# Performance work log

Hardware: AMD Instinct MI355X
Metric: run time of the kernel (lower is better)

Reference implementation:

```python
import jax, jax.numpy as jnp
import numpy as np

B, S, D = 4, 4096, 1024

def setup_inputs() -> dict:
    key = jax.random.key(0)
    kx, kq, kk, kv = jax.random.split(key, 4)
    x = jax.random.normal(kx, (B, S, D), dtype=jnp.float32)
    # nn.Linear weights, stored here as [d_in, d_out] so y = x @ W
    scale = 1.0 / np.sqrt(D)
    Wq = jax.random.normal(kq, (D, D), dtype=jnp.float32) * scale
    Wk = jax.random.normal(kk, (D, D), dtype=jnp.float32) * scale
    Wv = jax.random.normal(kv, (D, D), dtype=jnp.float32) * scale
    return {"x": x, "Wq": Wq, "Wk": Wk, "Wv": Wv}

def reference(x, Wq, Wk, Wv):
    b, n, d_in = x.shape
    d_out = Wk.shape[1]
    q = jnp.einsum('bnd,de->bne', x, Wq)
    k = jnp.einsum('bnd,de,->bne', x, Wk, 1.0)  # keys
    v = jnp.einsum('bnd,de->bne', x, Wv)
    # full causal attention: scores scaled by 1/sqrt(d_out) AFTER masking (matches source)
    scores = jnp.einsum('bqe,bke->bqk', q, k)
    causal = jnp.triu(jnp.ones((n, n), dtype=bool), k=1)  # True above diagonal -> masked
    scores = jnp.where(causal[None, :, :], -jnp.inf, scores)
    attn = jax.nn.softmax(scores / jnp.sqrt(jnp.asarray(d_out, scores.dtype)), axis=-1)
    # dropout p=0.0 (eval) -> identity
    return jnp.einsum('bqk,bke->bqe', attn, v)
```

## Files before the change

kernel.cpp:

```cpp
#include <hip/hip_runtime.h>
#include <hip/hip_bf16.h>

#define B_ 4
#define S_ 4096
#define D_ 1024
#define NT_ 32
#define PAIRS_ 528

typedef __attribute__((ext_vector_type(8))) short short8;
typedef __attribute__((ext_vector_type(4))) float f32x4;

__device__ __forceinline__ unsigned short f2bf(float f) {
    union { float f; unsigned u; } v; v.f = f;
    unsigned u = v.u;
    return (unsigned short)((u + 0x7fffu + ((u >> 16) & 1u)) >> 16);
}

__device__ __forceinline__ void gld_lds16(const unsigned short* g, unsigned short* l) {
    __builtin_amdgcn_global_load_lds((const __attribute__((address_space(1))) void*)g,
                                     (__attribute__((address_space(3))) void*)l, 16, 0, 0);
}

#define LGKM0 asm volatile("s_waitcnt lgkmcnt(0)" ::: "memory")
#define VM0   asm volatile("s_waitcnt vmcnt(0)" ::: "memory")
#define VM4   asm volatile("s_waitcnt vmcnt(4)" ::: "memory")
#define BAR   __builtin_amdgcn_s_barrier()
#define SB0   __builtin_amdgcn_sched_barrier(0)

__global__ __launch_bounds__(256) void prep_x(const float* __restrict__ x,
                                              unsigned short* __restrict__ xb) {
    size_t i = ((size_t)blockIdx.x * 256 + threadIdx.x) * 8;
    float4 a = *(const float4*)&x[i];
    float4 b = *(const float4*)&x[i + 4];
    unsigned u0 = (unsigned)f2bf(a.x) | ((unsigned)f2bf(a.y) << 16);
    unsigned u1 = (unsigned)f2bf(a.z) | ((unsigned)f2bf(a.w) << 16);
    unsigned u2 = (unsigned)f2bf(b.x) | ((unsigned)f2bf(b.y) << 16);
    unsigned u3 = (unsigned)f2bf(b.z) | ((unsigned)f2bf(b.w) << 16);
    uint4 val; val.x = u0; val.y = u1; val.z = u2; val.w = u3;
    *(uint4*)&xb[i] = val;
}

__global__ __launch_bounds__(256) void prep_w(const float* __restrict__ Wq,
                                              const float* __restrict__ Wk,
                                              const float* __restrict__ Wv,
                                              unsigned short* __restrict__ Wt) {
    __shared__ float ls[64 * 65];
    const int z = blockIdx.z;
    const float* __restrict__ W = (z == 0) ? Wq : (z == 1) ? Wk : Wv;
    unsigned short* __restrict__ Wtz = Wt + (size_t)z * D_ * D_;
    const int k0 = blockIdx.y * 64, n0 = blockIdx.x * 64;
    const int tid = threadIdx.x;
    #pragma unroll
    for (int i = 0; i < 16; ++i) {
        int lin = i * 256 + tid, r = lin >> 6, c = lin & 63;
        ls[r * 65 + c] = W[(size_t)(k0 + r) * D_ + n0 + c];
    }
    __syncthreads();
    #pragma unroll
    for (int i = 0; i < 16; ++i) {
        int lin = i * 256 + tid, r = lin >> 6, c = lin & 63;
        Wtz[(size_t)(n0 + r) * D_ + k0 + c] = f2bf(ls[c * 65 + r]);
    }
}

__global__ __launch_bounds__(512, 2) void qkv_gemm(
    const unsigned short* __restrict__ xb, const unsigned short* __restrict__ Wt,
    unsigned short* __restrict__ Q, unsigned short* __restrict__ K,
    unsigned short* __restrict__ Vt)
{
    __shared__ __align__(16) unsigned short ls[3 * 16384];

    const int z = blockIdx.z;
    const float scale = (z == 0) ? 0.03125f : 1.0f;

    const int lin = blockIdx.x;
    const int wg = (lin & 7) * 32 + (lin >> 3);
    const int m0 = (wg >> 2) * 256, n0 = (wg & 3) * 256;

    const int tid = threadIdx.x, lane = tid & 63, w = tid >> 6;
    const int wm = w >> 2, wn = w & 3;
    const int quad = lane >> 4, ln = lane & 15;

    const unsigned short* Ab = xb + (size_t)m0 * D_;
    const unsigned short* Bb = Wt + (size_t)z * D_ * D_ + (size_t)n0 * D_;

#define QKV_STAGE(kt, r)                                                          \
    {                                                                             \
        _Pragma("unroll")                                                         \
        for (int i_ = 0; i_ < 2; ++i_) {                                          \
            int g_ = tid + i_ * 512;                                              \
            int row_ = g_ >> 2;                                                   \
            int gs_ = (g_ & 3) ^ ((row_ >> 1) & 3);                               \
            gld_lds16(Ab + (size_t)row_ * D_ + (kt) * 32 + gs_ * 8,               \
                      ls + (r) * 16384 + g_ * 8);                                 \
            gld_lds16(Bb + (size_t)row_ * D_ + (kt) * 32 + gs_ * 8,               \
                      ls + (r) * 16384 + 8192 + g_ * 8);                          \
        }                                                                         \
    }

    f32x4 acc[8][4] = {};

#define QKV_BODY(r)                                                              \
    {                                                                            \
        const unsigned short* As_ = ls + (r) * 16384;                            \
        const unsigned short* Bs_ = As_ + 8192;                                  \
        short8 a_[8], b_[4];                                                     \
        _Pragma("unroll")                                                        \
        for (int mf_ = 0; mf_ < 8; ++mf_) {                                      \
            int row_ = wm * 128 + mf_ * 16 + ln;                                 \
            int g_ = quad ^ ((row_ >> 1) & 3);                                   \
            a_[mf_] = *(const short8*)&As_[row_ * 32 + g_ * 8];                  \
        }                                                                        \
        _Pragma("unroll")                                                        \
        for (int nf_ = 0; nf_ < 4; ++nf_) {                                      \
            int row_ = wn * 64 + nf_ * 16 + ln;                                  \
            int g_ = quad ^ ((row_ >> 1) & 3);                                   \
            b_[nf_] = *(const short8*)&Bs_[row_ * 32 + g_ * 8];                  \
        }                                                                        \
        __builtin_amdgcn_s_setprio(1);                                          \
        _Pragma("unroll")                                                        \
        for (int mf_ = 0; mf_ < 8; ++mf_)                                        \
            _Pragma("unroll")                                                    \
            for (int nf_ = 0; nf_ < 4; ++nf_)                                    \
                acc[mf_][nf_] = __builtin_amdgcn_mfma_f32_16x16x32_bf16(         \
                    a_[mf_], b_[nf_], acc[mf_][nf_], 0, 0, 0);                   \
        __builtin_amdgcn_s_setprio(0);                                          \
    }

#define QKV_STEP(t, r, rn, wcode)                                                \
    {                                                                            \
        if ((wcode) == 0) QKV_STAGE((t) + 2, rn)                                 \
        SB0;                                                                     \
        QKV_BODY(r)                                                              \
        LGKM0; SB0;                                                              \
        if ((wcode) == 0)      { VM4; SB0; BAR; SB0; }                           \
        else if ((wcode) == 1) { VM0; SB0; BAR; SB0; }                           \
    }

    QKV_STAGE(0, 0) QKV_STAGE(1, 1)
    VM4; SB0;
    BAR; SB0;

    #pragma unroll 1
    for (int tb = 0; tb < 30; tb += 3) {
        QKV_STEP(tb,     0, 2, 0)
        QKV_STEP(tb + 1, 1, 0, 0)
        QKV_STEP(tb + 2, 2, 1, 0)
    }
    QKV_STEP(30, 0, 0, 1)
    QKV_STEP(31, 1, 0, 2)

#undef QKV_STAGE
#undef QKV_BODY
#undef QKV_STEP

    if (z != 2) {
        unsigned short* __restrict__ Y = (z == 0) ? Q : K;
        #pragma unroll
        for (int mf = 0; mf < 8; ++mf)
            #pragma unroll
            for (int nf = 0; nf < 4; ++nf)
                #pragma unroll
                for (int rr = 0; rr < 4; ++rr) {
                    int row = m0 + wm * 128 + mf * 16 + quad * 4 + rr;
                    int col = n0 + wn * 64 + nf * 16 + ln;
                    Y[(size_t)row * D_ + col] = f2bf(acc[mf][nf][rr] * scale);
                }
    } else {
        BAR;
        unsigned int* U = (unsigned int*)ls + w * 2080;
        const int b_ = m0 >> 12;
        const int sbase = (m0 & 4095) + wm * 128;
        unsigned int* VtU = (unsigned int*)Vt;
        #pragma unroll
        for (int ch = 0; ch < 2; ++ch) {
            #pragma unroll
            for (int nfl = 0; nfl < 2; ++nfl) {
                int nf = ch * 2 + nfl;
                int el = nfl * 16 + ln;
                #pragma unroll
                for (int mf = 0; mf < 8; ++mf)
                    #pragma unroll
                    for (int pr = 0; pr < 2; ++pr) {
                        unsigned lo = f2bf(acc[mf][nf][2 * pr]);
                        unsigned hi = f2bf(acc[mf][nf][2 * pr + 1]);
                        U[el * 65 + mf * 8 + quad * 2 + pr] = lo | (hi << 16);
                    }
            }
            LGKM0; SB0;
            #pragma unroll 4
            for (int el = 0; el < 32; ++el) {
                unsigned v = U[el * 65 + lane];
                int eg = n0 + wn * 64 + ch * 32 + el;
                VtU[(((size_t)b_ * D_ + eg) * S_ + sbase) / 2 + lane] = v;
            }
            if (ch == 0) { LGKM0; SB0; }
        }
    }
}

__global__ __launch_bounds__(256, 3) void qk_pexp(
    const unsigned short* __restrict__ Q, const unsigned short* __restrict__ K,
    unsigned short* __restrict__ P, float* __restrict__ lpart)
{
    __shared__ __align__(16) unsigned short ls[3 * 8192];
    __shared__ float sml[2][128];

    const int l = blockIdx.x, b = blockIdx.y;
    const int r = l & 7;
    const int s = l >> 3;
    int qt, kt;
    if (s < r + 1)            { qt = r;      kt = s; }
    else if (s < 33)          { qt = 31 - r; kt = s - (r + 1); }
    else if (s < 42 + r)      { qt = 8 + r;  kt = s - 33; }
    else                      { qt = 23 - r; kt = s - (42 + r); }
    const int p = qt * (qt + 1) / 2 + kt;

    const int q0 = qt * 128, k0 = kt * 128;
    const int tid = threadIdx.x, lane = tid & 63, w = tid >> 6;
    const int wm = w >> 1, wn = w & 1, quad = lane >> 4, ln = lane & 15;
    const size_t base = (size_t)b * S_ * D_;

    const unsigned short* Qb = Q + base + (size_t)q0 * D_;
    const unsigned short* Kb = K + base + (size_t)k0 * D_;

#define QK_STAGE(kt_, r_)                                                         \
    {                                                                             \
        _Pragma("unroll")                                                         \
        for (int i_ = 0; i_ < 2; ++i_) {                                          \
            int g_ = tid + i_ * 256;                                              \
            int row_ = g_ >> 2;                                                   \
            int gs_ = (g_ & 3) ^ ((row_ >> 1) & 3);                               \
            gld_lds16(Qb + (size_t)row_ * D_ + (kt_) * 32 + gs_ * 8,              \
                      ls + (r_) * 8192 + g_ * 8);                                 \
            gld_lds16(Kb + (size_t)row_ * D_ + (kt_) * 32 + gs_ * 8,              \
                      ls + (r_) * 8192 + 4096 + g_ * 8);                          \
        }                                                                         \
    }

    f32x4 acc[4][4] = {};

#define QK_BODY(r_)                                                              \
    {                                                                            \
        const unsigned short* As_ = ls + (r_) * 8192;                            \
        const unsigned short* Bs_ = As_ + 4096;                                  \
        short8 a_[4], b_[4];                                                     \
        _Pragma("unroll")                                                        \
        for (int mf_ = 0; mf_ < 4; ++mf_) {                                      \
            int row_ = wm * 64 + mf_ * 16 + ln;                                  \
            int g_ = quad ^ ((row_ >> 1) & 3);                                   \
            a_[mf_] = *(const short8*)&As_[row_ * 32 + g_ * 8];                  \
        }                                                                        \
        _Pragma("unroll")                                                        \
        for (int nf_ = 0; nf_ < 4; ++nf_) {                                      \
            int row_ = wn * 64 + nf_ * 16 + ln;                                  \
            int g_ = quad ^ ((row_ >> 1) & 3);                                   \
            b_[nf_] = *(const short8*)&Bs_[row_ * 32 + g_ * 8];                  \
        }                                                                        \
        __builtin_amdgcn_s_setprio(1);                                          \
        _Pragma("unroll")                                                        \
        for (int mf_ = 0; mf_ < 4; ++mf_)                                        \
            _Pragma("unroll")                                                    \
            for (int nf_ = 0; nf_ < 4; ++nf_)                                    \
                acc[mf_][nf_] = __builtin_amdgcn_mfma_f32_16x16x32_bf16(         \
                    a_[mf_], b_[nf_], acc[mf_][nf_], 0, 0, 0);                   \
        __builtin_amdgcn_s_setprio(0);                                          \
    }

#define QK_STEP(t, r_, rn, wcode)                                                \
    {                                                                            \
        if ((wcode) == 0) QK_STAGE((t) + 2, rn)                                  \
        SB0;                                                                     \
        QK_BODY(r_)                                                              \
        LGKM0; SB0;                                                              \
        if ((wcode) == 0)      { VM4; SB0; BAR; SB0; }                           \
        else if ((wcode) == 1) { VM0; SB0; BAR; SB0; }                           \
    }

    QK_STAGE(0, 0) QK_STAGE(1, 1)
    VM4; SB0;
    BAR; SB0;

    #pragma unroll 1
    for (int tb = 0; tb < 30; tb += 3) {
        QK_STEP(tb,     0, 2, 0)
        QK_STEP(tb + 1, 1, 0, 0)
        QK_STEP(tb + 2, 2, 1, 0)
    }
    QK_STEP(30, 0, 0, 1)
    QK_STEP(31, 1, 0, 2)

#undef QK_STAGE
#undef QK_BODY
#undef QK_STEP

    const bool diag = (kt == qt);
    unsigned short* Pt = P + ((size_t)b * PAIRS_ + p) * (128 * 128);

    #pragma unroll
    for (int mf = 0; mf < 4; ++mf)
        #pragma unroll
        for (int rr = 0; rr < 4; ++rr) {
            int rowq = wm * 64 + mf * 16 + quad * 4 + rr;
            float lsum = 0.0f;
            #pragma unroll
            for (int nf = 0; nf < 4; ++nf) {
                int ckey = wn * 64 + nf * 16 + ln;
                float sc = acc[mf][nf][rr];
                float pe = (diag && ckey > rowq) ? 0.0f : __expf(fminf(sc, 60.0f));
                Pt[rowq * 128 + ckey] = f2bf(pe);
                lsum += pe;
            }
            #pragma unroll
            for (int off = 1; off < 16; off <<= 1)
                lsum += __shfl_xor(lsum, off);
            if (ln == 0) sml[wn][rowq] = lsum;
        }
    __syncthreads();

    if (tid < 128)
        lpart[((size_t)b * PAIRS_ + p) * 128 + tid] = sml[0][tid] + sml[1][tid];
}

__global__ __launch_bounds__(128) void merge_il(const float* __restrict__ lpart,
                                                float* __restrict__ il) {
    const int qt = blockIdx.x, b = blockIdx.y;
    const int row = threadIdx.x;
    const int pbase = qt * (qt + 1) / 2;
    float l = 0.0f;
    for (int kt = 0; kt <= qt; ++kt)
        l += lpart[((size_t)b * PAIRS_ + pbase + kt) * 128 + row];
    il[(size_t)b * S_ + qt * 128 + row] = 1.0f / l;
}

__global__ __launch_bounds__(256, 3) void pv_gemm(
    const unsigned short* __restrict__ P, const unsigned short* __restrict__ Vt,
    const float* __restrict__ il, float* __restrict__ O)
{
    __shared__ __align__(16) unsigned short ls[3 * 8192];

    const int bid = blockIdx.x;
    const int u  = (bid & 7) | ((bid >> 6) << 3);
    const int dt = (bid >> 3) & 7;
    const int pair = u & 15;
    const int b = u >> 4;
    const int d0 = dt * 128;
    const int tid = threadIdx.x, lane = tid & 63, w = tid >> 6;
    const int wm = w >> 1, wn = w & 1, quad = lane >> 4, ln = lane & 15;

    const unsigned short* Vtb = Vt + ((size_t)b * D_ + d0) * S_;

#define PV_STAGE(c_, r_)                                                          \
    {                                                                             \
        const unsigned short* Pt_ = Pbase + (size_t)((c_) >> 2) * (128 * 128);    \
        _Pragma("unroll")                                                         \
        for (int i_ = 0; i_ < 2; ++i_) {                                          \
            int g_ = tid + i_ * 256;                                              \
            int row_ = g_ >> 2;                                                   \
            int gs_ = (g_ & 3) ^ ((row_ >> 1) & 3);                               \
            gld_lds16(Pt_ + (size_t)row_ * 128 + ((c_) & 3) * 32 + gs_ * 8,       \
                      ls + (r_) * 8192 + g_ * 8);                                 \
            gld_lds16(Vtb + (size_t)row_ * S_ + (c_) * 32 + gs_ * 8,              \
                      ls + (r_) * 8192 + 4096 + g_ * 8);                          \
        }                                                                         \
    }

#define PV_BODY(r_)                                                              \
    {                                                                            \
        const unsigned short* As_ = ls + (r_) * 8192;                            \
        const unsigned short* Bs_ = As_ + 4096;                                  \
        short8 a_[4], b_[4];                                                     \
        _Pragma("unroll")                                                        \
        for (int mf_ = 0; mf_ < 4; ++mf_) {                                      \
            int row_ = wm * 64 + mf_ * 16 + ln;                                  \
            int g_ = quad ^ ((row_ >> 1) & 3);                                   \
            a_[mf_] = *(const short8*)&As_[row_ * 32 + g_ * 8];                  \
        }                                                                        \
        _Pragma("unroll")                                                        \
        for (int nf_ = 0; nf_ < 4; ++nf_) {                                      \
            int row_ = wn * 64 + nf_ * 16 + ln;                                  \
            int g_ = quad ^ ((row_ >> 1) & 3);                                   \
            b_[nf_] = *(const short8*)&Bs_[row_ * 32 + g_ * 8];                  \
        }                                                                        \
        __builtin_amdgcn_s_setprio(1);                                          \
        _Pragma("unroll")                                                        \
        for (int mf_ = 0; mf_ < 4; ++mf_)                                        \
            _Pragma("unroll")                                                    \
            for (int nf_ = 0; nf_ < 4; ++nf_)                                    \
                acc[mf_][nf_] = __builtin_amdgcn_mfma_f32_16x16x32_bf16(         \
                    a_[mf_], b_[nf_], acc[mf_][nf_], 0, 0, 0);                   \
        __builtin_amdgcn_s_setprio(0);                                          \
    }

    #pragma unroll 1
    for (int half = 0; half < 2; ++half) {
        const int qt = half ? pair : (31 - pair);
        const int q0 = qt * 128;
        const int pbase = qt * (qt + 1) / 2;
        const int nst = 4 * (qt + 1);
        const unsigned short* Pbase = P + ((size_t)b * PAIRS_ + pbase) * (128 * 128);

        f32x4 acc[4][4] = {};

        if (half) { BAR; SB0; }
        PV_STAGE(0, 0) PV_STAGE(1, 1)
        VM4; SB0;
        BAR; SB0;

        #pragma unroll 1
        for (int t = 0; t < nst; ++t) {
            const int r_ = t % 3;
            if (t + 2 < nst) { const int rn_ = (t + 2) % 3; PV_STAGE(t + 2, rn_) }
            SB0;
            PV_BODY(r_)
            LGKM0; SB0;
            if (t + 2 < nst)      { VM4; SB0; }
            else if (t + 1 < nst) { VM0; SB0; }
            if (t + 1 < nst) { BAR; SB0; }
        }

        #pragma unroll
        for (int mf = 0; mf < 4; ++mf) {
            float ilv[4];
            #pragma unroll
            for (int rr = 0; rr < 4; ++rr)
                ilv[rr] = il[(size_t)b * S_ + q0 + wm * 64 + mf * 16 + quad * 4 + rr];
            #pragma unroll
            for (int nf = 0; nf < 4; ++nf)
                #pragma unroll
                for (int rr = 0; rr < 4; ++rr) {
                    int rowq = q0 + wm * 64 + mf * 16 + quad * 4 + rr;
                    int col = d0 + wn * 64 + nf * 16 + ln;
                    O[((size_t)b * S_ + rowq) * D_ + col] = acc[mf][nf][rr] * ilv[rr];
                }
        }
    }
#undef PV_STAGE
#undef PV_BODY
}

extern "C" void kernel_launch(void* const* d_in, const int* in_sizes, int n_in,
                              void* d_out, int out_size, void* d_ws, size_t ws_size,
                              hipStream_t stream) {
    const float* x  = (const float*)d_in[0];
    const float* Wq = (const float*)d_in[1];
    const float* Wk = (const float*)d_in[2];
    const float* Wv = (const float*)d_in[3];

    const size_t nQ = (size_t)B_ * S_ * D_;
    const size_t nP = (size_t)B_ * PAIRS_ * 128 * 128;

    unsigned short* P  = (unsigned short*)d_ws;
    unsigned short* xb = P;
    unsigned short* Q  = P + nP;
    unsigned short* K  = Q + nQ;
    unsigned short* Vt = K + nQ;
    unsigned short* Wt = Vt + nQ;
    float* lpart = (float*)(Wt + (size_t)3 * D_ * D_);
    float* il    = lpart + (size_t)B_ * PAIRS_ * 128;
    float* O = (float*)d_out;

    hipLaunchKernelGGL(prep_x, dim3(8192), dim3(256), 0, stream, x, xb);
    hipLaunchKernelGGL(prep_w, dim3(16, 16, 3), dim3(256), 0, stream, Wq, Wk, Wv, Wt);
    hipLaunchKernelGGL(qkv_gemm, dim3(256, 1, 3), dim3(512), 0, stream, xb, Wt, Q, K, Vt);
    hipLaunchKernelGGL(qk_pexp, dim3(PAIRS_, B_), dim3(256), 0, stream, Q, K, P, lpart);
    hipLaunchKernelGGL(merge_il, dim3(NT_, B_), dim3(128), 0, stream, lpart, il);
    hipLaunchKernelGGL(pv_gemm, dim3(512), dim3(256), 0, stream, P, Vt, il, O);
}
```

Baseline: 423.7 us.

## Compute two key tiles per block in QK^T to reuse Q tile loads

The QK score kernel now has most blocks compute a 128x256 score tile, covering two adjacent key tiles for one query tile, instead of 128x128. Diagonal tiles are handled by a separate square-tile path. This halves Q reloads from global memory and cuts the block count from 528 to 272 per batch. In exchange it uses more LDS and registers per block, with launch bounds lowered to 2 blocks per CU, and adds more complex tile-index mapping.

```diff
diff --git a/kernel.cpp b/kernel.cpp
--- a/kernel.cpp
+++ b/kernel.cpp
@@ -24,6 +24,7 @@
 #define LGKM0 asm volatile("s_waitcnt lgkmcnt(0)" ::: "memory")
 #define VM0   asm volatile("s_waitcnt vmcnt(0)" ::: "memory")
 #define VM4   asm volatile("s_waitcnt vmcnt(4)" ::: "memory")
+#define VM6   asm volatile("s_waitcnt vmcnt(6)" ::: "memory")
 #define BAR   __builtin_amdgcn_s_barrier()
 #define SB0   __builtin_amdgcn_sched_barrier(0)
 
@@ -199,50 +200,164 @@
     }
 }
 
-__global__ __launch_bounds__(256, 3) void qk_pexp(
+__global__ __launch_bounds__(256, 2) void qk_pexp(
     const unsigned short* __restrict__ Q, const unsigned short* __restrict__ K,
     unsigned short* __restrict__ P, float* __restrict__ lpart)
 {
-    __shared__ __align__(16) unsigned short ls[3 * 8192];
+    __shared__ __align__(16) unsigned short ls[3 * 12288];
     __shared__ float sml[2][128];
 
     const int l = blockIdx.x, b = blockIdx.y;
     const int r = l & 7;
     const int s = l >> 3;
-    int qt, kt;
-    if (s < r + 1)            { qt = r;      kt = s; }
-    else if (s < 33)          { qt = 31 - r; kt = s - (r + 1); }
-    else if (s < 42 + r)      { qt = 8 + r;  kt = s - 33; }
-    else                      { qt = 23 - r; kt = s - (42 + r); }
-    const int p = qt * (qt + 1) / 2 + kt;
-
-    const int q0 = qt * 128, k0 = kt * 128;
+    const size_t base = (size_t)b * S_ * D_;
     const int tid = threadIdx.x, lane = tid & 63, w = tid >> 6;
     const int wm = w >> 1, wn = w & 1, quad = lane >> 4, ln = lane & 15;
-    const size_t base = (size_t)b * S_ * D_;
-
-    const unsigned short* Qb = Q + base + (size_t)q0 * D_;
-    const unsigned short* Kb = K + base + (size_t)k0 * D_;
-
-#define QK_STAGE(kt_, r_)                                                         \
+
+    if (s < 32) {
+        const int qts0 = r, qts1 = 31 - r, qts2 = 8 + r, qts3 = 23 - r;
+        int qt = -1, j = 0, rem = s;
+        {
+            int np;
+            np = (qts0 + 1) >> 1; if (rem < np) { qt = qts0; j = rem; } rem -= np;
+            np = (qts1 + 1) >> 1; if (qt < 0 && rem < np) { qt = qts1; j = rem; } if (qt < 0) rem -= np;
+            np = (qts2 + 1) >> 1; if (qt < 0 && rem < np) { qt = qts2; j = rem; } if (qt < 0) rem -= np;
+            if (qt < 0) { qt = qts3; j = rem; }
+        }
+        const int q0 = qt * 128;
+        const int p0 = qt * (qt + 1) / 2 + 2 * j;
+        const unsigned short* Qb  = Q + base + (size_t)q0 * D_;
+        const unsigned short* Kb2 = K + base + (size_t)(j * 256) * D_;
+
+#define QP_STAGE(c_, r_)                                                          \
     {                                                                             \
         _Pragma("unroll")                                                         \
         for (int i_ = 0; i_ < 2; ++i_) {                                          \
             int g_ = tid + i_ * 256;                                              \
             int row_ = g_ >> 2;                                                   \
             int gs_ = (g_ & 3) ^ ((row_ >> 1) & 3);                               \
-            gld_lds16(Qb + (size_t)row_ * D_ + (kt_) * 32 + gs_ * 8,              \
-                      ls + (r_) * 8192 + g_ * 8);                                 \
-            gld_lds16(Kb + (size_t)row_ * D_ + (kt_) * 32 + gs_ * 8,              \
-                      ls + (r_) * 8192 + 4096 + g_ * 8);                          \
+            gld_lds16(Qb + (size_t)row_ * D_ + (c_) * 32 + gs_ * 8,               \
+                      ls + (r_) * 12288 + g_ * 8);                                \
         }                                                                         \
-    }
-
-    f32x4 acc[4][4] = {};
-
-#define QK_BODY(r_)                                                              \
-    {                                                                            \
-        const unsigned short* As_ = ls + (r_) * 8192;                            \
+        _Pragma("unroll")                                                         \
+        for (int i_ = 0; i_ < 4; ++i_) {                                          \
+            int g_ = tid + i_ * 256;                                              \
+            int row_ = g_ >> 2;                                                   \
+            int gs_ = (g_ & 3) ^ ((row_ >> 1) & 3);                               \
+            gld_lds16(Kb2 + (size_t)row_ * D_ + (c_) * 32 + gs_ * 8,              \
+                      ls + (r_) * 12288 + 4096 + g_ * 8);                         \
+        }                                                                         \
+    }
+
+        f32x4 acc[4][8] = {};
+
+#define QP_BODY(r_)                                                              \
+    {                                                                            \
+        const unsigned short* As_ = ls + (r_) * 12288;                           \
+        const unsigned short* Bs_ = As_ + 4096;                                  \
+        short8 a_[4], b_[8];                                                     \
+        _Pragma("unroll")                                                        \
+        for (int mf_ = 0; mf_ < 4; ++mf_) {                                      \
+            int row_ = wm * 64 + mf_ * 16 + ln;                                  \
+            int g_ = quad ^ ((row_ >> 1) & 3);                                   \
+            a_[mf_] = *(const short8*)&As_[row_ * 32 + g_ * 8];                  \
+        }                                                                        \
+        _Pragma("unroll")                                                        \
+        for (int nf_ = 0; nf_ < 8; ++nf_) {                                      \
+            int row_ = wn * 128 + nf_ * 16 + ln;                                 \
+            int g_ = quad ^ ((row_ >> 1) & 3);                                   \
+            b_[nf_] = *(const short8*)&Bs_[row_ * 32 + g_ * 8];                  \
+        }                                                                        \
+        __builtin_amdgcn_s_setprio(1);                                          \
+        _Pragma("unroll")                                                        \
+        for (int mf_ = 0; mf_ < 4; ++mf_)                                        \
+            _Pragma("unroll")                                                    \
+            for (int nf_ = 0; nf_ < 8; ++nf_)                                    \
+                acc[mf_][nf_] = __builtin_amdgcn_mfma_f32_16x16x32_bf16(         \
+                    a_[mf_], b_[nf_], acc[mf_][nf_], 0, 0, 0);                   \
+        __builtin_amdgcn_s_setprio(0);                                          \
+    }
+
+#define QP_STEP(t, r_, rn, wcode)                                                \
+    {                                                                            \
+        if ((wcode) == 0) QP_STAGE((t) + 2, rn)                                  \
+        SB0;                                                                     \
+        QP_BODY(r_)                                                              \
+        LGKM0; SB0;                                                              \
+        if ((wcode) == 0)      { VM6; SB0; BAR; SB0; }                           \
+        else if ((wcode) == 1) { VM0; SB0; BAR; SB0; }                           \
+    }
+
+        QP_STAGE(0, 0) QP_STAGE(1, 1)
+        VM6; SB0;
+        BAR; SB0;
+
+        #pragma unroll 1
+        for (int tb = 0; tb < 30; tb += 3) {
+            QP_STEP(tb,     0, 2, 0)
+            QP_STEP(tb + 1, 1, 0, 0)
+            QP_STEP(tb + 2, 2, 1, 0)
+        }
+        QP_STEP(30, 0, 0, 1)
+        QP_STEP(31, 1, 0, 2)
+
+#undef QP_STAGE
+#undef QP_BODY
+#undef QP_STEP
+
+        const bool mt = (2 * j + 1 == qt) && (wn == 1);
+        unsigned short* Pt = P + ((size_t)b * PAIRS_ + p0 + wn) * (128 * 128);
+        #pragma unroll
+        for (int mf = 0; mf < 4; ++mf)
+            #pragma unroll
+            for (int rr = 0; rr < 4; ++rr) {
+                int rowq = wm * 64 + mf * 16 + quad * 4 + rr;
+                float lsum = 0.0f;
+                #pragma unroll
+                for (int nf = 0; nf < 8; ++nf) {
+                    int ckey = nf * 16 + ln;
+                    float sc = acc[mf][nf][rr];
+                    float pe = (mt && ckey > rowq) ? 0.0f : __expf(fminf(sc, 60.0f));
+                    Pt[rowq * 128 + ckey] = f2bf(pe);
+                    lsum += pe;
+                }
+                #pragma unroll
+                for (int off = 1; off < 16; off <<= 1)
+                    lsum += __shfl_xor(lsum, off);
+                if (ln == 0) sml[wn][rowq] = lsum;
+            }
+        __syncthreads();
+        if (tid < 128) {
+            lpart[((size_t)b * PAIRS_ + p0) * 128 + tid]     = sml[0][tid];
+            lpart[((size_t)b * PAIRS_ + p0 + 1) * 128 + tid] = sml[1][tid];
+        }
+    } else {
+        const int qt = (r & 1) ? ((s == 32) ? 31 - r : 23 - r)
+                               : ((s == 32) ? r : 8 + r);
+        const int q0 = qt * 128;
+        const int p = qt * (qt + 1) / 2 + qt;
+        const unsigned short* Qb = Q + base + (size_t)q0 * D_;
+        const unsigned short* Kb = K + base + (size_t)q0 * D_;
+
+#define QS_STAGE(c_, r_)                                                          \
+    {                                                                             \
+        _Pragma("unroll")                                                         \
+        for (int i_ = 0; i_ < 2; ++i_) {                                          \
+            int g_ = tid + i_ * 256;                                              \
+            int row_ = g_ >> 2;                                                   \
+            int gs_ = (g_ & 3) ^ ((row_ >> 1) & 3);                               \
+            gld_lds16(Qb + (size_t)row_ * D_ + (c_) * 32 + gs_ * 8,               \
+                      ls + (r_) * 12288 + g_ * 8);                                \
+            gld_lds16(Kb + (size_t)row_ * D_ + (c_) * 32 + gs_ * 8,               \
+                      ls + (r_) * 12288 + 4096 + g_ * 8);                         \
+        }                                                                         \
+    }
+
+        f32x4 acc[4][4] = {};
+
+#define QS_BODY(r_)                                                              \
+    {                                                                            \
+        const unsigned short* As_ = ls + (r_) * 12288;                           \
         const unsigned short* Bs_ = As_ + 4096;                                  \
         short8 a_[4], b_[4];                                                     \
         _Pragma("unroll")                                                        \
@@ -267,59 +382,57 @@
         __builtin_amdgcn_s_setprio(0);                                          \
     }
 
-#define QK_STEP(t, r_, rn, wcode)                                                \
-    {                                                                            \
-        if ((wcode) == 0) QK_STAGE((t) + 2, rn)                                  \
+#define QS_STEP(t, r_, rn, wcode)                                                \
+    {                                                                            \
+        if ((wcode) == 0) QS_STAGE((t) + 2, rn)                                  \
         SB0;                                                                     \
-        QK_BODY(r_)                                                              \
+        QS_BODY(r_)                                                              \
         LGKM0; SB0;                                                              \
         if ((wcode) == 0)      { VM4; SB0; BAR; SB0; }                           \
         else if ((wcode) == 1) { VM0; SB0; BAR; SB0; }                           \
     }
 
-    QK_STAGE(0, 0) QK_STAGE(1, 1)
-    VM4; SB0;
-    BAR; SB0;
-
-    #pragma unroll 1
-    for (int tb = 0; tb < 30; tb += 3) {
-        QK_STEP(tb,     0, 2, 0)
-        QK_STEP(tb + 1, 1, 0, 0)
-        QK_STEP(tb + 2, 2, 1, 0)
-    }
-    QK_STEP(30, 0, 0, 1)
-    QK_STEP(31, 1, 0, 2)
-
-#undef QK_STAGE
-#undef QK_BODY
-#undef QK_STEP
-
-    const bool diag = (kt == qt);
-    unsigned short* Pt = P + ((size_t)b * PAIRS_ + p) * (128 * 128);
-
-    #pragma unroll
-    for (int mf = 0; mf < 4; ++mf)
+        QS_STAGE(0, 0) QS_STAGE(1, 1)
+        VM4; SB0;
+        BAR; SB0;
+
+        #pragma unroll 1
+        for (int tb = 0; tb < 30; tb += 3) {
+            QS_STEP(tb,     0, 2, 0)
+            QS_STEP(tb + 1, 1, 0, 0)
+            QS_STEP(tb + 2, 2, 1, 0)
+        }
+        QS_STEP(30, 0, 0, 1)
+        QS_STEP(31, 1, 0, 2)
+
+#undef QS_STAGE
+#undef QS_BODY
+#undef QS_STEP
+
+        unsigned short* Pt = P + ((size_t)b * PAIRS_ + p) * (128 * 128);
         #pragma unroll
-        for (int rr = 0; rr < 4; ++rr) {
-            int rowq = wm * 64 + mf * 16 + quad * 4 + rr;
-            float lsum = 0.0f;
+        for (int mf = 0; mf < 4; ++mf)
             #pragma unroll
-            for (int nf = 0; nf < 4; ++nf) {
-                int ckey = wn * 64 + nf * 16 + ln;
-                float sc = acc[mf][nf][rr];
-                float pe = (diag && ckey > rowq) ? 0.0f : __expf(fminf(sc, 60.0f));
-                Pt[rowq * 128 + ckey] = f2bf(pe);
-                lsum += pe;
+            for (int rr = 0; rr < 4; ++rr) {
+                int rowq = wm * 64 + mf * 16 + quad * 4 + rr;
+                float lsum = 0.0f;
+                #pragma unroll
+                for (int nf = 0; nf < 4; ++nf) {
+                    int ckey = wn * 64 + nf * 16 + ln;
+                    float sc = acc[mf][nf][rr];
+                    float pe = (ckey > rowq) ? 0.0f : __expf(fminf(sc, 60.0f));
+                    Pt[rowq * 128 + ckey] = f2bf(pe);
+                    lsum += pe;
+                }
+                #pragma unroll
+                for (int off = 1; off < 16; off <<= 1)
+                    lsum += __shfl_xor(lsum, off);
+                if (ln == 0) sml[wn][rowq] = lsum;
             }
-            #pragma unroll
-            for (int off = 1; off < 16; off <<= 1)
-                lsum += __shfl_xor(lsum, off);
-            if (ln == 0) sml[wn][rowq] = lsum;
-        }
-    __syncthreads();
-
-    if (tid < 128)
-        lpart[((size_t)b * PAIRS_ + p) * 128 + tid] = sml[0][tid] + sml[1][tid];
+        __syncthreads();
+        if (tid < 128)
+            lpart[((size_t)b * PAIRS_ + p) * 128 + tid] = sml[0][tid] + sml[1][tid];
+    }
 }
 
 __global__ __launch_bounds__(128) void merge_il(const float* __restrict__ lpart,
@@ -463,7 +576,7 @@
     hipLaunchKernelGGL(prep_x, dim3(8192), dim3(256), 0, stream, x, xb);
     hipLaunchKernelGGL(prep_w, dim3(16, 16, 3), dim3(256), 0, stream, Wq, Wk, Wv, Wt);
     hipLaunchKernelGGL(qkv_gemm, dim3(256, 1, 3), dim3(512), 0, stream, xb, Wt, Q, K, Vt);
-    hipLaunchKernelGGL(qk_pexp, dim3(PAIRS_, B_), dim3(256), 0, stream, Q, K, P, lpart);
+    hipLaunchKernelGGL(qk_pexp, dim3(272, B_), dim3(256), 0, stream, Q, K, P, lpart);
     hipLaunchKernelGGL(merge_il, dim3(NT_, B_), dim3(128), 0, stream, lpart, il);
     hipLaunchKernelGGL(pv_gemm, dim3(512), dim3(256), 0, stream, P, Vt, il, O);
 }
```

Result: faster. 405.2 us (-4.4%).
